# Kernel tuning notes

Hardware: AMD Instinct MI355X
Metric: run time of the kernel (lower is better)

The kernel has to match this reference:

```python
import jax, jax.numpy as jnp
import numpy as np

N, D = 2048, 1024
H, KV, HD = 16, 4, 64
REPEATS = H // KV
SCALE = HD ** -0.5


def setup_inputs() -> dict:
    key = jax.random.key(0)
    ks = jax.random.split(key, 6)
    x = jax.random.normal(ks[0], (N, D), dtype=jnp.float32)
    # rotary tables: cos/sin of interleaved-pair angles (llama-style view_as_complex)
    pos = jnp.arange(N, dtype=jnp.float32)[:, None]
    inv_freq = 1.0 / (10000.0 ** (jnp.arange(0, HD, 2, dtype=jnp.float32) / HD))
    ang = pos * inv_freq[None, :]  # (N, HD//2)
    freqs_cos = jnp.cos(ang)
    freqs_sin = jnp.sin(ang)
    s = 0.02
    Wq = jax.random.normal(ks[1], (D, H * HD), dtype=jnp.float32) * s
    Wk = jax.random.normal(ks[2], (D, KV * HD), dtype=jnp.float32) * s
    Wv = jax.random.normal(ks[3], (D, KV * HD), dtype=jnp.float32) * s
    Wo = jax.random.normal(ks[4], (H * HD, D), dtype=jnp.float32) * s
    return {"x": x, "freqs_cos": freqs_cos, "freqs_sin": freqs_sin,
            "Wq": Wq, "Wk": Wk, "Wv": Wv, "Wo": Wo}


def _rope(t, cos, sin):
    # t: (N, heads, HD); interleaved complex pairs (even=real, odd=imag)
    tr = t[..., 0::2]
    ti = t[..., 1::2]
    c = cos[:, None, :]
    s = sin[:, None, :]
    out_r = tr * c - ti * s
    out_i = tr * s + ti * c
    return jnp.stack([out_r, out_i], axis=-1).reshape(t.shape)


def reference(x, freqs_cos, freqs_sin, Wq, Wk, Wv, Wo):
    n = x.shape[0]
    xq = (x @ Wq).reshape(n, H, HD)
    xk = (x @ Wk).reshape(n, KV, HD)
    xv = (x @ Wv).reshape(n, KV, HD)
    xq = _rope(xq, freqs_cos, freqs_sin)
    xk = _rope(xk, freqs_cos, freqs_sin)
    # repeat_kv along head dim (GQA)
    k = jnp.repeat(xk, REPEATS, axis=1)  # (n, H, HD)
    v = jnp.repeat(xv, REPEATS, axis=1)
    # memory_efficient_attention with mask=None: full attention over token axis
    scores = jnp.einsum('nhd,mhd->hnm', xq, k) * SCALE
    attn = jax.nn.softmax(scores, axis=-1)
    out = jnp.einsum('hnm,mhd->nhd', attn, v)
    return out.reshape(n, H * HD) @ Wo
```

## Files before the change

### kernel.cpp

```cpp
#include <hip/hip_runtime.h>

#define N_TOK 2048
#define DMODEL 1024
#define NH 16
#define NKV 4
#define HDIM 64
#define SCALE_LOG2E 0.1803368801111204f

typedef __attribute__((ext_vector_type(8))) short short8;
typedef __attribute__((ext_vector_type(4))) float f32x4;
typedef __attribute__((ext_vector_type(16))) float f32x16;
typedef unsigned short u16;
typedef unsigned int u32;

__device__ __forceinline__ u16 f2bf(float x) {
    u32 u = __float_as_uint(x);
    u += 0x7FFF + ((u >> 16) & 1);
    return (u16)(u >> 16);
}
__device__ __forceinline__ u32 pack2(float a, float b) {
    return (u32)f2bf(a) | ((u32)f2bf(b) << 16);
}
__device__ __forceinline__ u32 pack2t(float a, float b) {
    return __builtin_amdgcn_perm(__float_as_uint(b), __float_as_uint(a), 0x07060302u);
}

__global__ __launch_bounds__(256) void prep(
    const float* __restrict__ Wq, const float* __restrict__ Wk,
    const float* __restrict__ Wv, const float* __restrict__ Wo,
    const float* __restrict__ x,
    u16* __restrict__ Wqt, u16* __restrict__ Wkt, u16* __restrict__ Wvt,
    u16* __restrict__ Wot, u16* __restrict__ xb)
{
    const int z = blockIdx.z;
    const int t = threadIdx.x;
    if (z == 4) {
        size_t base = ((size_t)(blockIdx.y * 16 + blockIdx.x)) * 8192;
#pragma unroll
        for (int i = 0; i < 8; ++i) {
            float4 v = *(const float4*)(x + base + i * 1024 + t * 4);
            uint2 p; p.x = pack2(v.x, v.y); p.y = pack2(v.z, v.w);
            *(uint2*)(xb + base + i * 1024 + t * 4) = p;
        }
        return;
    }
    const float* W; u16* Wt; int NC;
    if      (z == 0) { W = Wq; Wt = Wqt; NC = 1024; }
    else if (z == 1) { W = Wk; Wt = Wkt; NC = 256; }
    else if (z == 2) { W = Wv; Wt = Wvt; NC = 256; }
    else             { W = Wo; Wt = Wot; NC = 1024; }
    const int n0 = blockIdx.x * 64;
    if (n0 >= NC) return;
    const int k0 = blockIdx.y * 64;
    __shared__ float T[64][68];
    const int row = t >> 2, cs = (t & 3) * 16;
#pragma unroll
    for (int i = 0; i < 4; ++i)
        *(float4*)&T[row][cs + i * 4] =
            *(const float4*)(W + (size_t)(k0 + row) * NC + n0 + cs + i * 4);
    __syncthreads();
    const int nl = t >> 2, ks = (t & 3) * 16;
    u32 pk[8];
#pragma unroll
    for (int i = 0; i < 8; ++i)
        pk[i] = pack2(T[ks + 2 * i][nl], T[ks + 2 * i + 1][nl]);
    u16* dst = Wt + (size_t)(n0 + nl) * DMODEL + k0 + ks;
    uint4 w0; w0.x = pk[0]; w0.y = pk[1]; w0.z = pk[2]; w0.w = pk[3];
    uint4 w1; w1.x = pk[4]; w1.y = pk[5]; w1.z = pk[6]; w1.w = pk[7];
    *(uint4*)(dst) = w0;
    *(uint4*)(dst + 8) = w1;
}

__global__ __launch_bounds__(256, 2) void gemm_qkv(
    const u16* __restrict__ A,
    const u16* __restrict__ B0, const u16* __restrict__ B1, const u16* __restrict__ B2,
    u16* __restrict__ D0, u16* __restrict__ D1, u16* __restrict__ FVout,
    const float* __restrict__ fc, const float* __restrict__ fs)
{
    __shared__ u16 As[2][128][72];
    __shared__ u16 Bs[2][64][72];
    const int t = threadIdx.x;
    const int m0 = blockIdx.x * 128;
    const int by = blockIdx.y;

    const u16* Bt; int nl0, ep;
    u16* dbf = nullptr; int dstride = 0; float epsc = 1.f;
    if (by < 16)      { Bt = B0; nl0 = by * 64;        dbf = D0; ep = 1; dstride = 1024;
                        epsc = SCALE_LOG2E; }
    else if (by < 20) { Bt = B1; nl0 = (by - 16) * 64; dbf = D1; ep = 1; dstride = 256; }
    else              { Bt = B2; nl0 = (by - 20) * 64; ep = 2; }

    const int w = t >> 6, lane = t & 63;
    const int quad = lane >> 4, l15 = lane & 15;
    const int wm = (w >> 1) * 64, wn = (w & 1) * 32;
    const int arow = t >> 1, ac = (t & 1) * 32;
    const int brow = t >> 2, bc = (t & 3) * 16;

    const u16* Ap = A + (size_t)(m0 + arow) * DMODEL + ac;
    const u16* Bp = Bt + (size_t)(nl0 + brow) * DMODEL + bc;

    f32x4 acc[4][2];
#pragma unroll
    for (int i = 0; i < 4; ++i)
#pragma unroll
        for (int j = 0; j < 2; ++j) acc[i][j] = {0.f, 0.f, 0.f, 0.f};

    uint4 a_r[4], b_r[2];
#pragma unroll
    for (int ci = 0; ci < 4; ++ci) a_r[ci] = *(const uint4*)(Ap + ci * 8);
    b_r[0] = *(const uint4*)(Bp);
    b_r[1] = *(const uint4*)(Bp + 8);
#pragma unroll
    for (int ci = 0; ci < 4; ++ci) *(uint4*)&As[0][arow][ac + ci * 8] = a_r[ci];
    *(uint4*)&Bs[0][brow][bc]     = b_r[0];
    *(uint4*)&Bs[0][brow][bc + 8] = b_r[1];
    __syncthreads();

    for (int it = 0; it < 16; ++it) {
        const int cur = it & 1;
        const bool more = (it + 1) < 16;
        if (more) {
            const int k1 = (it + 1) * 64;
#pragma unroll
            for (int ci = 0; ci < 4; ++ci) a_r[ci] = *(const uint4*)(Ap + k1 + ci * 8);
            b_r[0] = *(const uint4*)(Bp + k1);
            b_r[1] = *(const uint4*)(Bp + k1 + 8);
        }
#pragma unroll
        for (int c = 0; c < 2; ++c) {
            short8 af[4], bf[2];
#pragma unroll
            for (int i = 0; i < 4; ++i)
                af[i] = *(const short8*)&As[cur][wm + i * 16 + l15][c * 32 + quad * 8];
#pragma unroll
            for (int j = 0; j < 2; ++j)
                bf[j] = *(const short8*)&Bs[cur][wn + j * 16 + l15][c * 32 + quad * 8];
#pragma unroll
            for (int i = 0; i < 4; ++i)
#pragma unroll
                for (int j = 0; j < 2; ++j)
                    acc[i][j] = __builtin_amdgcn_mfma_f32_16x16x32_bf16(af[i], bf[j], acc[i][j], 0, 0, 0);
        }
        if (more) {
            const int nx = cur ^ 1;
#pragma unroll
            for (int ci = 0; ci < 4; ++ci) *(uint4*)&As[nx][arow][ac + ci * 8] = a_r[ci];
            *(uint4*)&Bs[nx][brow][bc]     = b_r[0];
            *(uint4*)&Bs[nx][brow][bc + 8] = b_r[1];
            __syncthreads();
        }
    }

#pragma unroll
    for (int i = 0; i < 4; ++i)
#pragma unroll
        for (int j = 0; j < 2; ++j) {
            const int cl = nl0 + wn + j * 16 + l15;
            if (ep == 1) {
#pragma unroll
                for (int r4 = 0; r4 < 4; ++r4) {
                    const int r = m0 + wm + i * 16 + quad * 4 + r4;
                    float own = acc[i][j][r4];
                    float other = __shfl_xor(own, 1, 64);
                    const int p = (cl & 63) >> 1;
                    const float c = fc[r * 32 + p] * epsc, s = fs[r * 32 + p] * epsc;
                    float outv = ((cl & 1) == 0) ? (own * c - other * s)
                                                 : (other * s + own * c);
                    dbf[(size_t)r * dstride + cl] = f2bf(outv);
                }
            } else {
                const int rb = m0 + wm + i * 16 + quad * 4;
                const int g = cl >> 6, d = cl & 63;
                const int d2 = d >> 5, dl = d & 31;
                const int keyblk = rb >> 7, kg = (rb >> 5) & 3;
                const int kst = (rb >> 4) & 1, hb = (rb >> 3) & 1, jv = rb & 7;
                size_t idx = ((((((size_t)(g * 16 + keyblk) * 4 + kg) * 2 + kst) * 2 + d2)
                               * 2 + hb) * 32 + dl) * 8 + jv;
                uint2 pk;
                pk.x = pack2(acc[i][j][0], acc[i][j][1]);
                pk.y = pack2(acc[i][j][2], acc[i][j][3]);
                *(uint2*)(FVout + idx) = pk;
            }
        }
}

__global__ __launch_bounds__(256, 2) void gemm_out(
    const u16* __restrict__ A, const u16* __restrict__ Bt, float* __restrict__ Dout)
{
    __shared__ u16 As[2][64][72];
    __shared__ u16 Bs[2][64][72];
    const int t = threadIdx.x;
    const int m0 = blockIdx.x * 64;
    const int nl0 = blockIdx.y * 64;

    const int w = t >> 6, lane = t & 63;
    const int quad = lane >> 4, l15 = lane & 15;
    const int wm = (w >> 1) * 32, wn = (w & 1) * 32;
    const int srow = t >> 2, sk = (t & 3) * 16;

    const u16* Ap = A + (size_t)(m0 + srow) * DMODEL + sk;
    const u16* Bp = Bt + (size_t)(nl0 + srow) * DMODEL + sk;

    f32x4 acc[2][2];
#pragma unroll
    for (int i = 0; i < 2; ++i)
#pragma unroll
        for (int j = 0; j < 2; ++j) acc[i][j] = {0.f, 0.f, 0.f, 0.f};

    uint4 a_r[2], b_r[2];
    a_r[0] = *(const uint4*)(Ap);     a_r[1] = *(const uint4*)(Ap + 8);
    b_r[0] = *(const uint4*)(Bp);     b_r[1] = *(const uint4*)(Bp + 8);
    *(uint4*)&As[0][srow][sk]     = a_r[0];
    *(uint4*)&As[0][srow][sk + 8] = a_r[1];
    *(uint4*)&Bs[0][srow][sk]     = b_r[0];
    *(uint4*)&Bs[0][srow][sk + 8] = b_r[1];
    __syncthreads();

    for (int it = 0; it < 16; ++it) {
        const int cur = it & 1;
        const bool more = (it + 1) < 16;
        if (more) {
            const int k1 = (it + 1) * 64;
            a_r[0] = *(const uint4*)(Ap + k1);     a_r[1] = *(const uint4*)(Ap + k1 + 8);
            b_r[0] = *(const uint4*)(Bp + k1);     b_r[1] = *(const uint4*)(Bp + k1 + 8);
        }
#pragma unroll
        for (int c = 0; c < 2; ++c) {
            short8 af[2], bf[2];
#pragma unroll
            for (int i = 0; i < 2; ++i)
                af[i] = *(const short8*)&As[cur][wm + i * 16 + l15][c * 32 + quad * 8];
#pragma unroll
            for (int j = 0; j < 2; ++j)
                bf[j] = *(const short8*)&Bs[cur][wn + j * 16 + l15][c * 32 + quad * 8];
#pragma unroll
            for (int i = 0; i < 2; ++i)
#pragma unroll
                for (int j = 0; j < 2; ++j)
                    acc[i][j] = __builtin_amdgcn_mfma_f32_16x16x32_bf16(af[i], bf[j], acc[i][j], 0, 0, 0);
        }
        if (more) {
            const int nx = cur ^ 1;
            *(uint4*)&As[nx][srow][sk]     = a_r[0];
            *(uint4*)&As[nx][srow][sk + 8] = a_r[1];
            *(uint4*)&Bs[nx][srow][sk]     = b_r[0];
            *(uint4*)&Bs[nx][srow][sk + 8] = b_r[1];
            __syncthreads();
        }
    }

#pragma unroll
    for (int i = 0; i < 2; ++i)
#pragma unroll
        for (int j = 0; j < 2; ++j) {
            const int cl = nl0 + wn + j * 16 + l15;
#pragma unroll
            for (int r4 = 0; r4 < 4; ++r4) {
                const int r = m0 + wm + i * 16 + quad * 4 + r4;
                Dout[(size_t)r * 1024 + cl] = acc[i][j][r4];
            }
        }
}

__global__ __launch_bounds__(256, 2) void attn(
    const u16* __restrict__ Qb, const u16* __restrict__ Kb,
    const u16* __restrict__ FV, u16* __restrict__ Ob)
{
    __shared__ u16 Ks[2][2][64][72];
    __shared__ u16 Ps[4][32][40];

    const int t = threadIdx.x;
    const int n0 = blockIdx.x * 64;
    const int h = blockIdx.y, kvh = h >> 2;
    const int w = t >> 6, lane = t & 63;
    const int hi = lane >> 5, l31 = lane & 31;
    const int qgrp = w & 1, khalf = w >> 1;
    const int srow = t >> 1, ssel = (t & 1) * 32;
    const int khalf_s = srow >> 6, klocal = srow & 63;

    const short8 ones = {(short)0x3F80, (short)0x3F80, (short)0x3F80, (short)0x3F80,
                         (short)0x3F80, (short)0x3F80, (short)0x3F80, (short)0x3F80};

    const u16* qp = Qb + (size_t)(n0 + qgrp * 32 + l31) * (NH * HDIM) + h * HDIM + hi * 8;
    short8 qf[4];
#pragma unroll
    for (int s = 0; s < 4; ++s) qf[s] = *(const short8*)(qp + s * 16);

    const u16* kbase = Kb + (size_t)(khalf_s * 1024 + klocal) * (NKV * HDIM) + kvh * HDIM + ssel;
    const u16* fvb = FV + ((size_t)kvh * 16 * 8192) + (size_t)lane * 8;

    f32x16 o[2], o_l;
#pragma unroll
    for (int d2 = 0; d2 < 2; ++d2)
#pragma unroll
        for (int r = 0; r < 16; ++r) o[d2][r] = 0.f;
#pragma unroll
    for (int r = 0; r < 16; ++r) o_l[r] = 0.f;

#pragma unroll
    for (int c = 0; c < 4; ++c)
        *(uint4*)&Ks[0][khalf_s][klocal][ssel + c * 8] = *(const uint4*)(kbase + c * 8);
    __syncthreads();

    for (int rd = 0; rd < 16; ++rd) {
        const int cur = rd & 1, nxt = cur ^ 1;
        const int rdn = (rd + 1) & 15;
        uint4 kr[4];
#pragma unroll
        for (int c = 0; c < 4; ++c)
            kr[c] = *(const uint4*)(kbase + (size_t)(rdn * 64) * (NKV * HDIM) + c * 8);

#pragma unroll
        for (int kg = 0; kg < 2; ++kg) {
            const int kg_global = khalf * 32 + rd * 2 + kg;
            const int keyblk = kg_global >> 2, kgi = kg_global & 3;
            short8 vf[2][2];
#pragma unroll
            for (int s = 0; s < 2; ++s)
#pragma unroll
                for (int d2 = 0; d2 < 2; ++d2)
                    vf[s][d2] = *(const short8*)(fvb +
                        ((((size_t)keyblk * 4 + kgi) * 2 + s) * 2 + d2) * 512);
            f32x16 sa;
#pragma unroll
            for (int r = 0; r < 16; ++r) sa[r] = 0.f;
#pragma unroll
            for (int s = 0; s < 4; ++s) {
                short8 kf = *(const short8*)&Ks[cur][khalf][kg * 32 + l31][s * 16 + hi * 8];
                sa = __builtin_amdgcn_mfma_f32_32x32x16_bf16(kf, qf[s], sa, 0, 0, 0);
            }
            float p[16];
#pragma unroll
            for (int r = 0; r < 16; ++r) p[r] = __builtin_amdgcn_exp2f(sa[r]);
#pragma unroll
            for (int blk = 0; blk < 4; ++blk) {
                uint2 pk;
                pk.x = pack2t(p[blk * 4 + 0], p[blk * 4 + 1]);
                pk.y = pack2t(p[blk * 4 + 2], p[blk * 4 + 3]);
                *(uint2*)&Ps[w][l31][blk * 8 + 4 * hi] = pk;
            }
            const short8 ap0 = *(const short8*)&Ps[w][l31][hi * 8];
            const short8 ap1 = *(const short8*)&Ps[w][l31][16 + hi * 8];
#pragma unroll
            for (int d2 = 0; d2 < 2; ++d2) {
                o[d2] = __builtin_amdgcn_mfma_f32_32x32x16_bf16(ap0, vf[0][d2], o[d2], 0, 0, 0);
                o[d2] = __builtin_amdgcn_mfma_f32_32x32x16_bf16(ap1, vf[1][d2], o[d2], 0, 0, 0);
            }
            o_l = __builtin_amdgcn_mfma_f32_32x32x16_bf16(ap0, ones, o_l, 0, 0, 0);
            o_l = __builtin_amdgcn_mfma_f32_32x32x16_bf16(ap1, ones, o_l, 0, 0, 0);
        }
#pragma unroll
        for (int c = 0; c < 4; ++c)
            *(uint4*)&Ks[nxt][khalf_s][klocal][ssel + c * 8] = kr[c];
        __syncthreads();
    }

    float* Xf = (float*)&Ks[0][0][0][0];
    if (khalf == 1) {
#pragma unroll
        for (int d2 = 0; d2 < 2; ++d2)
#pragma unroll
            for (int r = 0; r < 16; ++r) {
                const int q32 = (r & 3) + 8 * (r >> 2) + 4 * hi;
                Xf[qgrp * 2048 + q32 * 64 + d2 * 32 + l31] = o[d2][r];
            }
        if (l31 == 0) {
#pragma unroll
            for (int r = 0; r < 16; ++r) {
                const int q32 = (r & 3) + 8 * (r >> 2) + 4 * hi;
                Xf[4096 + qgrp * 32 + q32] = o_l[r];
            }
        }
    }
    __syncthreads();
    if (khalf == 0) {
        float linv[16];
#pragma unroll
        for (int r = 0; r < 16; ++r) {
            const int q32 = (r & 3) + 8 * (r >> 2) + 4 * hi;
            linv[r] = 1.f / (o_l[r] + Xf[4096 + qgrp * 32 + q32]);
        }
#pragma unroll
        for (int d2 = 0; d2 < 2; ++d2)
#pragma unroll
            for (int r = 0; r < 16; ++r) {
                const int q32 = (r & 3) + 8 * (r >> 2) + 4 * hi;
                const float val = o[d2][r] + Xf[qgrp * 2048 + q32 * 64 + d2 * 32 + l31];
                const int qrow = n0 + qgrp * 32 + q32;
                Ob[(size_t)qrow * (NH * HDIM) + h * HDIM + d2 * 32 + l31] = f2bf(val * linv[r]);
            }
    }
}

extern "C" void kernel_launch(void* const* d_in, const int* in_sizes, int n_in,
                              void* d_out, int out_size, void* d_ws, size_t ws_size,
                              hipStream_t stream) {
    const float* x  = (const float*)d_in[0];
    const float* fc = (const float*)d_in[1];
    const float* fs = (const float*)d_in[2];
    const float* Wq = (const float*)d_in[3];
    const float* Wk = (const float*)d_in[4];
    const float* Wv = (const float*)d_in[5];
    const float* Wo = (const float*)d_in[6];
    float* out = (float*)d_out;

    u16* ws  = (u16*)d_ws;
    u16* xb  = ws;
    u16* Wqt = xb  + (size_t)2048 * 1024;
    u16* Wkt = Wqt + (size_t)1024 * 1024;
    u16* Wvt = Wkt + (size_t)256 * 1024;
    u16* Wot = Wvt + (size_t)256 * 1024;
    u16* qb  = Wot + (size_t)1024 * 1024;
    u16* kb  = qb  + (size_t)2048 * 1024;
    u16* fv  = kb  + (size_t)2048 * 256;
    u16* aob = fv  + (size_t)256 * 2048;

    prep<<<dim3(16, 16, 5), dim3(256), 0, stream>>>(Wq, Wk, Wv, Wo, x,
                                                    Wqt, Wkt, Wvt, Wot, xb);
    gemm_qkv<<<dim3(16, 24), dim3(256), 0, stream>>>(xb, Wqt, Wkt, Wvt,
                                                     qb, kb, fv, fc, fs);
    attn<<<dim3(32, 16), dim3(256), 0, stream>>>(qb, kb, fv, aob);
    gemm_out<<<dim3(32, 16), dim3(256), 0, stream>>>(aob, Wot, out);
}
```

Baseline: 137.2 us.

## Fuse four kernels into one persistent kernel with grid-wide barriers

Measured after the change: 350.7 us. +155.5%, slower.

```diff
diff --git a/kernel.cpp b/kernel.cpp
--- a/kernel.cpp
+++ b/kernel.cpp
@@ -6,6 +6,7 @@
 #define NKV 4
 #define HDIM 64
 #define SCALE_LOG2E 0.1803368801111204f
+#define NBLK 512
 
 typedef __attribute__((ext_vector_type(8))) short short8;
 typedef __attribute__((ext_vector_type(4))) float f32x4;
@@ -25,369 +26,382 @@
     return __builtin_amdgcn_perm(__float_as_uint(b), __float_as_uint(a), 0x07060302u);
 }
 
-__global__ __launch_bounds__(256) void prep(
+__device__ __forceinline__ void gridbar(u32* cnt, u32* gen) {
+    __syncthreads();
+    if (threadIdx.x == 0) {
+        __threadfence();
+        u32 g = __hip_atomic_load(gen, __ATOMIC_RELAXED, __HIP_MEMORY_SCOPE_AGENT);
+        if (__hip_atomic_fetch_add(cnt, 1u, __ATOMIC_ACQ_REL, __HIP_MEMORY_SCOPE_AGENT)
+            == (u32)(NBLK - 1)) {
+            __hip_atomic_store(cnt, 0u, __ATOMIC_RELAXED, __HIP_MEMORY_SCOPE_AGENT);
+            __hip_atomic_fetch_add(gen, 1u, __ATOMIC_RELEASE, __HIP_MEMORY_SCOPE_AGENT);
+        } else {
+            while (__hip_atomic_load(gen, __ATOMIC_RELAXED, __HIP_MEMORY_SCOPE_AGENT) == g)
+                __builtin_amdgcn_s_sleep(2);
+        }
+        __threadfence();
+    }
+    __syncthreads();
+}
+
+__global__ __launch_bounds__(256, 2) void fused(
+    const float* __restrict__ x, const float* __restrict__ fc, const float* __restrict__ fs,
     const float* __restrict__ Wq, const float* __restrict__ Wk,
     const float* __restrict__ Wv, const float* __restrict__ Wo,
-    const float* __restrict__ x,
-    u16* __restrict__ Wqt, u16* __restrict__ Wkt, u16* __restrict__ Wvt,
-    u16* __restrict__ Wot, u16* __restrict__ xb)
+    u16* __restrict__ xb, u16* __restrict__ Wqt, u16* __restrict__ Wkt,
+    u16* __restrict__ Wvt, u16* __restrict__ Wot,
+    u16* __restrict__ qb, u16* __restrict__ kb, u16* __restrict__ fv,
+    u16* __restrict__ aob, float* __restrict__ out, u32* __restrict__ sync)
 {
-    const int z = blockIdx.z;
+    __shared__ __align__(16) unsigned char smem[55296];
+    const int b = blockIdx.x;
     const int t = threadIdx.x;
-    if (z == 4) {
-        size_t base = ((size_t)(blockIdx.y * 16 + blockIdx.x)) * 8192;
-#pragma unroll
-        for (int i = 0; i < 8; ++i) {
-            float4 v = *(const float4*)(x + base + i * 1024 + t * 4);
-            uint2 p; p.x = pack2(v.x, v.y); p.y = pack2(v.z, v.w);
-            *(uint2*)(xb + base + i * 1024 + t * 4) = p;
-        }
-        return;
+
+    for (int job = b; job < 896; job += NBLK) {
+        if (job < 256) {
+            size_t base = (size_t)job * 8192;
+#pragma unroll
+            for (int i = 0; i < 8; ++i) {
+                float4 v = *(const float4*)(x + base + i * 1024 + t * 4);
+                uint2 p; p.x = pack2(v.x, v.y); p.y = pack2(v.z, v.w);
+                *(uint2*)(xb + base + i * 1024 + t * 4) = p;
+            }
+        } else {
+            const float* W; u16* Wt; int NC, jr;
+            if (job < 512)      { W = Wq; Wt = Wqt; NC = 1024; jr = job - 256; }
+            else if (job < 768) { W = Wo; Wt = Wot; NC = 1024; jr = job - 512; }
+            else if (job < 832) { W = Wk; Wt = Wkt; NC = 256;  jr = job - 768; }
+            else                { W = Wv; Wt = Wvt; NC = 256;  jr = job - 832; }
+            const int n0 = (NC == 1024 ? (jr & 15) : (jr & 3)) * 64;
+            const int k0 = (NC == 1024 ? (jr >> 4) : (jr >> 2)) * 64;
+            float (*T)[68] = (float(*)[68])smem;
+            const int row = t >> 2, cs = (t & 3) * 16;
+#pragma unroll
+            for (int i = 0; i < 4; ++i)
+                *(float4*)&T[row][cs + i * 4] =
+                    *(const float4*)(W + (size_t)(k0 + row) * NC + n0 + cs + i * 4);
+            __syncthreads();
+            const int nl = t >> 2, ks = (t & 3) * 16;
+            u32 pk[8];
+#pragma unroll
+            for (int i = 0; i < 8; ++i)
+                pk[i] = pack2(T[ks + 2 * i][nl], T[ks + 2 * i + 1][nl]);
+            u16* dst = Wt + (size_t)(n0 + nl) * DMODEL + k0 + ks;
+            uint4 w0; w0.x = pk[0]; w0.y = pk[1]; w0.z = pk[2]; w0.w = pk[3];
+            uint4 w1; w1.x = pk[4]; w1.y = pk[5]; w1.z = pk[6]; w1.w = pk[7];
+            *(uint4*)(dst) = w0;
+            *(uint4*)(dst + 8) = w1;
+            __syncthreads();
+        }
     }
-    const float* W; u16* Wt; int NC;
-    if      (z == 0) { W = Wq; Wt = Wqt; NC = 1024; }
-    else if (z == 1) { W = Wk; Wt = Wkt; NC = 256; }
-    else if (z == 2) { W = Wv; Wt = Wvt; NC = 256; }
-    else             { W = Wo; Wt = Wot; NC = 1024; }
-    const int n0 = blockIdx.x * 64;
-    if (n0 >= NC) return;
-    const int k0 = blockIdx.y * 64;
-    __shared__ float T[64][68];
-    const int row = t >> 2, cs = (t & 3) * 16;
-#pragma unroll
-    for (int i = 0; i < 4; ++i)
-        *(float4*)&T[row][cs + i * 4] =
-            *(const float4*)(W + (size_t)(k0 + row) * NC + n0 + cs + i * 4);
-    __syncthreads();
-    const int nl = t >> 2, ks = (t & 3) * 16;
-    u32 pk[8];
-#pragma unroll
-    for (int i = 0; i < 8; ++i)
-        pk[i] = pack2(T[ks + 2 * i][nl], T[ks + 2 * i + 1][nl]);
-    u16* dst = Wt + (size_t)(n0 + nl) * DMODEL + k0 + ks;
-    uint4 w0; w0.x = pk[0]; w0.y = pk[1]; w0.z = pk[2]; w0.w = pk[3];
-    uint4 w1; w1.x = pk[4]; w1.y = pk[5]; w1.z = pk[6]; w1.w = pk[7];
-    *(uint4*)(dst) = w0;
-    *(uint4*)(dst + 8) = w1;
-}
-
-__global__ __launch_bounds__(256, 2) void gemm_qkv(
-    const u16* __restrict__ A,
-    const u16* __restrict__ B0, const u16* __restrict__ B1, const u16* __restrict__ B2,
-    u16* __restrict__ D0, u16* __restrict__ D1, u16* __restrict__ FVout,
-    const float* __restrict__ fc, const float* __restrict__ fs)
-{
-    __shared__ u16 As[2][128][72];
-    __shared__ u16 Bs[2][64][72];
-    const int t = threadIdx.x;
-    const int m0 = blockIdx.x * 128;
-    const int by = blockIdx.y;
-
-    const u16* Bt; int nl0, ep;
-    u16* dbf = nullptr; int dstride = 0; float epsc = 1.f;
-    if (by < 16)      { Bt = B0; nl0 = by * 64;        dbf = D0; ep = 1; dstride = 1024;
-                        epsc = SCALE_LOG2E; }
-    else if (by < 20) { Bt = B1; nl0 = (by - 16) * 64; dbf = D1; ep = 1; dstride = 256; }
-    else              { Bt = B2; nl0 = (by - 20) * 64; ep = 2; }
-
-    const int w = t >> 6, lane = t & 63;
-    const int quad = lane >> 4, l15 = lane & 15;
-    const int wm = (w >> 1) * 64, wn = (w & 1) * 32;
-    const int arow = t >> 1, ac = (t & 1) * 32;
-    const int brow = t >> 2, bc = (t & 3) * 16;
-
-    const u16* Ap = A + (size_t)(m0 + arow) * DMODEL + ac;
-    const u16* Bp = Bt + (size_t)(nl0 + brow) * DMODEL + bc;
-
-    f32x4 acc[4][2];
-#pragma unroll
-    for (int i = 0; i < 4; ++i)
-#pragma unroll
-        for (int j = 0; j < 2; ++j) acc[i][j] = {0.f, 0.f, 0.f, 0.f};
-
-    uint4 a_r[4], b_r[2];
-#pragma unroll
-    for (int ci = 0; ci < 4; ++ci) a_r[ci] = *(const uint4*)(Ap + ci * 8);
-    b_r[0] = *(const uint4*)(Bp);
-    b_r[1] = *(const uint4*)(Bp + 8);
-#pragma unroll
-    for (int ci = 0; ci < 4; ++ci) *(uint4*)&As[0][arow][ac + ci * 8] = a_r[ci];
-    *(uint4*)&Bs[0][brow][bc]     = b_r[0];
-    *(uint4*)&Bs[0][brow][bc + 8] = b_r[1];
-    __syncthreads();
-
-    for (int it = 0; it < 16; ++it) {
-        const int cur = it & 1;
-        const bool more = (it + 1) < 16;
-        if (more) {
-            const int k1 = (it + 1) * 64;
-#pragma unroll
-            for (int ci = 0; ci < 4; ++ci) a_r[ci] = *(const uint4*)(Ap + k1 + ci * 8);
-            b_r[0] = *(const uint4*)(Bp + k1);
-            b_r[1] = *(const uint4*)(Bp + k1 + 8);
-        }
-#pragma unroll
-        for (int c = 0; c < 2; ++c) {
-            short8 af[4], bf[2];
-#pragma unroll
-            for (int i = 0; i < 4; ++i)
-                af[i] = *(const short8*)&As[cur][wm + i * 16 + l15][c * 32 + quad * 8];
-#pragma unroll
-            for (int j = 0; j < 2; ++j)
-                bf[j] = *(const short8*)&Bs[cur][wn + j * 16 + l15][c * 32 + quad * 8];
-#pragma unroll
-            for (int i = 0; i < 4; ++i)
+    gridbar(sync, sync + 16);
+
+    if (b < 384) {
+        u16 (*As)[128][72] = (u16(*)[128][72])smem;
+        u16 (*Bs)[64][72]  = (u16(*)[64][72])(smem + 36864);
+        const int m0 = (b & 15) * 128;
+        const int by = b >> 4;
+
+        const u16* Bt; int nl0, ep;
+        u16* dbf = nullptr; int dstride = 0; float epsc = 1.f;
+        if (by < 16)      { Bt = Wqt; nl0 = by * 64;        dbf = qb; ep = 1; dstride = 1024;
+                            epsc = SCALE_LOG2E; }
+        else if (by < 20) { Bt = Wkt; nl0 = (by - 16) * 64; dbf = kb; ep = 1; dstride = 256; }
+        else              { Bt = Wvt; nl0 = (by - 20) * 64; ep = 2; }
+
+        const int w = t >> 6, lane = t & 63;
+        const int quad = lane >> 4, l15 = lane & 15;
+        const int wm = (w >> 1) * 64, wn = (w & 1) * 32;
+        const int arow = t >> 1, ac = (t & 1) * 32;
+        const int brow = t >> 2, bc = (t & 3) * 16;
+
+        const u16* Ap = xb + (size_t)(m0 + arow) * DMODEL + ac;
+        const u16* Bp = Bt + (size_t)(nl0 + brow) * DMODEL + bc;
+
+        f32x4 acc[4][2];
+#pragma unroll
+        for (int i = 0; i < 4; ++i)
+#pragma unroll
+            for (int j = 0; j < 2; ++j) acc[i][j] = {0.f, 0.f, 0.f, 0.f};
+
+        uint4 a_r[4], b_r[2];
+#pragma unroll
+        for (int ci = 0; ci < 4; ++ci) a_r[ci] = *(const uint4*)(Ap + ci * 8);
+        b_r[0] = *(const uint4*)(Bp);
+        b_r[1] = *(const uint4*)(Bp + 8);
+#pragma unroll
+        for (int ci = 0; ci < 4; ++ci) *(uint4*)&As[0][arow][ac + ci * 8] = a_r[ci];
+        *(uint4*)&Bs[0][brow][bc]     = b_r[0];
+        *(uint4*)&Bs[0][brow][bc + 8] = b_r[1];
+        __syncthreads();
+
+        for (int it = 0; it < 16; ++it) {
+            const int cur = it & 1;
+            const bool more = (it + 1) < 16;
+            if (more) {
+                const int k1 = (it + 1) * 64;
+#pragma unroll
+                for (int ci = 0; ci < 4; ++ci) a_r[ci] = *(const uint4*)(Ap + k1 + ci * 8);
+                b_r[0] = *(const uint4*)(Bp + k1);
+                b_r[1] = *(const uint4*)(Bp + k1 + 8);
+            }
+#pragma unroll
+            for (int c = 0; c < 2; ++c) {
+                short8 af[4], bf[2];
+#pragma unroll
+                for (int i = 0; i < 4; ++i)
+                    af[i] = *(const short8*)&As[cur][wm + i * 16 + l15][c * 32 + quad * 8];
 #pragma unroll
                 for (int j = 0; j < 2; ++j)
-                    acc[i][j] = __builtin_amdgcn_mfma_f32_16x16x32_bf16(af[i], bf[j], acc[i][j], 0, 0, 0);
-        }
-        if (more) {
-            const int nx = cur ^ 1;
-#pragma unroll
-            for (int ci = 0; ci < 4; ++ci) *(uint4*)&As[nx][arow][ac + ci * 8] = a_r[ci];
-            *(uint4*)&Bs[nx][brow][bc]     = b_r[0];
-            *(uint4*)&Bs[nx][brow][bc + 8] = b_r[1];
+                    bf[j] = *(const short8*)&Bs[cur][wn + j * 16 + l15][c * 32 + quad * 8];
+#pragma unroll
+                for (int i = 0; i < 4; ++i)
+#pragma unroll
+                    for (int j = 0; j < 2; ++j)
+                        acc[i][j] = __builtin_amdgcn_mfma_f32_16x16x32_bf16(af[i], bf[j], acc[i][j], 0, 0, 0);
+            }
+            if (more) {
+                const int nx = cur ^ 1;
+#pragma unroll
+                for (int ci = 0; ci < 4; ++ci) *(uint4*)&As[nx][arow][ac + ci * 8] = a_r[ci];
+                *(uint4*)&Bs[nx][brow][bc]     = b_r[0];
+                *(uint4*)&Bs[nx][brow][bc + 8] = b_r[1];
+                __syncthreads();
+            }
+        }
+
+#pragma unroll
+        for (int i = 0; i < 4; ++i)
+#pragma unroll
+            for (int j = 0; j < 2; ++j) {
+                const int cl = nl0 + wn + j * 16 + l15;
+                if (ep == 1) {
+#pragma unroll
+                    for (int r4 = 0; r4 < 4; ++r4) {
+                        const int r = m0 + wm + i * 16 + quad * 4 + r4;
+                        float own = acc[i][j][r4];
+                        float other = __shfl_xor(own, 1, 64);
+                        const int p = (cl & 63) >> 1;
+                        const float c = fc[r * 32 + p] * epsc, s = fs[r * 32 + p] * epsc;
+                        float outv = ((cl & 1) == 0) ? (own * c - other * s)
+                                                     : (other * s + own * c);
+                        dbf[(size_t)r * dstride + cl] = f2bf(outv);
+                    }
+                } else {
+                    const int rb = m0 + wm + i * 16 + quad * 4;
+                    const int g = cl >> 6, d = cl & 63;
+                    const int d2 = d >> 5, dl = d & 31;
+                    const int keyblk = rb >> 7, kg = (rb >> 5) & 3;
+                    const int kst = (rb >> 4) & 1, hb = (rb >> 3) & 1, jv = rb & 7;
+                    size_t idx = ((((((size_t)(g * 16 + keyblk) * 4 + kg) * 2 + kst) * 2 + d2)
+                                   * 2 + hb) * 32 + dl) * 8 + jv;
+                    uint2 pk;
+                    pk.x = pack2(acc[i][j][0], acc[i][j][1]);
+                    pk.y = pack2(acc[i][j][2], acc[i][j][3]);
+                    *(uint2*)(fv + idx) = pk;
+                }
+            }
+    }
+    gridbar(sync, sync + 16);
+
+    {
+        u16 (*Ks)[2][64][72] = (u16(*)[2][64][72])smem;
+        u16 (*Ps)[32][40]    = (u16(*)[32][40])(smem + 36864);
+        const int n0 = (b & 31) * 64;
+        const int h = b >> 5, kvh = h >> 2;
+        const int w = t >> 6, lane = t & 63;
+        const int hi = lane >> 5, l31 = lane & 31;
+        const int qgrp = w & 1, khalf = w >> 1;
+        const int srow = t >> 1, ssel = (t & 1) * 32;
+        const int khalf_s = srow >> 6, klocal = srow & 63;
+
+        const short8 ones = {(short)0x3F80, (short)0x3F80, (short)0x3F80, (short)0x3F80,
+                             (short)0x3F80, (short)0x3F80, (short)0x3F80, (short)0x3F80};
+
+        const u16* qp = qb + (size_t)(n0 + qgrp * 32 + l31) * (NH * HDIM) + h * HDIM + hi * 8;
+        short8 qf[4];
+#pragma unroll
+        for (int s = 0; s < 4; ++s) qf[s] = *(const short8*)(qp + s * 16);
+
+        const u16* kbase = kb + (size_t)(khalf_s * 1024 + klocal) * (NKV * HDIM) + kvh * HDIM + ssel;
+        const u16* fvb = fv + ((size_t)kvh * 16 * 8192) + (size_t)lane * 8;
+
+        f32x16 o[2], o_l;
+#pragma unroll
+        for (int d2 = 0; d2 < 2; ++d2)
+#pragma unroll
+            for (int r = 0; r < 16; ++r) o[d2][r] = 0.f;
+#pragma unroll
+        for (int r = 0; r < 16; ++r) o_l[r] = 0.f;
+
+#pragma unroll
+        for (int c = 0; c < 4; ++c)
+            *(uint4*)&Ks[0][khalf_s][klocal][ssel + c * 8] = *(const uint4*)(kbase + c * 8);
+        __syncthreads();
+
+        for (int rd = 0; rd < 16; ++rd) {
+            const int cur = rd & 1, nxt = cur ^ 1;
+            const int rdn = (rd + 1) & 15;
+            uint4 kr[4];
+#pragma unroll
+            for (int c = 0; c < 4; ++c)
+                kr[c] = *(const uint4*)(kbase + (size_t)(rdn * 64) * (NKV * HDIM) + c * 8);
+
+#pragma unroll
+            for (int kg = 0; kg < 2; ++kg) {
+                const int kg_global = khalf * 32 + rd * 2 + kg;
+                const int keyblk = kg_global >> 2, kgi = kg_global & 3;
+                short8 vf[2][2];
+#pragma unroll
+                for (int s = 0; s < 2; ++s)
+#pragma unroll
+                    for (int d2 = 0; d2 < 2; ++d2)
+                        vf[s][d2] = *(const short8*)(fvb +
+                            ((((size_t)keyblk * 4 + kgi) * 2 + s) * 2 + d2) * 512);
+                f32x16 sa;
+#pragma unroll
+                for (int r = 0; r < 16; ++r) sa[r] = 0.f;
+#pragma unroll
+                for (int s = 0; s < 4; ++s) {
+                    short8 kf = *(const short8*)&Ks[cur][khalf][kg * 32 + l31][s * 16 + hi * 8];
+                    sa = __builtin_amdgcn_mfma_f32_32x32x16_bf16(kf, qf[s], sa, 0, 0, 0);
+                }
+                float p[16];
+#pragma unroll
+                for (int r = 0; r < 16; ++r) p[r] = __builtin_amdgcn_exp2f(sa[r]);
+#pragma unroll
+                for (int blk = 0; blk < 4; ++blk) {
+                    uint2 pk;
+                    pk.x = pack2t(p[blk * 4 + 0], p[blk * 4 + 1]);
+                    pk.y = pack2t(p[blk * 4 + 2], p[blk * 4 + 3]);
+                    *(uint2*)&Ps[w][l31][blk * 8 + 4 * hi] = pk;
+                }
+                const short8 ap0 = *(const short8*)&Ps[w][l31][hi * 8];
+                const short8 ap1 = *(const short8*)&Ps[w][l31][16 + hi * 8];
+#pragma unroll
+                for (int d2 = 0; d2 < 2; ++d2) {
+                    o[d2] = __builtin_amdgcn_mfma_f32_32x32x16_bf16(ap0, vf[0][d2], o[d2], 0, 0, 0);
+                    o[d2] = __builtin_amdgcn_mfma_f32_32x32x16_bf16(ap1, vf[1][d2], o[d2], 0, 0, 0);
+                }
+                o_l = __builtin_amdgcn_mfma_f32_32x32x16_bf16(ap0, ones, o_l, 0, 0, 0);
+                o_l = __builtin_amdgcn_mfma_f32_32x32x16_bf16(ap1, ones, o_l, 0, 0, 0);
+            }
+#pragma unroll
+            for (int c = 0; c < 4; ++c)
+                *(uint4*)&Ks[nxt][khalf_s][klocal][ssel + c * 8] = kr[c];
             __syncthreads();
         }
+
+        float* Xf = (float*)smem;
+        if (khalf == 1) {
+#pragma unroll
+            for (int d2 = 0; d2 < 2; ++d2)
+#pragma unroll
+                for (int r = 0; r < 16; ++r) {
+                    const int q32 = (r & 3) + 8 * (r >> 2) + 4 * hi;
+                    Xf[qgrp * 2048 + q32 * 64 + d2 * 32 + l31] = o[d2][r];
+                }
+            if (l31 == 0) {
+#pragma unroll
+                for (int r = 0; r < 16; ++r) {
+                    const int q32 = (r & 3) + 8 * (r >> 2) + 4 * hi;
+                    Xf[4096 + qgrp * 32 + q32] = o_l[r];
+                }
+            }
+        }
+        __syncthreads();
+        if (khalf == 0) {
+            float linv[16];
+#pragma unroll
+            for (int r = 0; r < 16; ++r) {
+                const int q32 = (r & 3) + 8 * (r >> 2) + 4 * hi;
+                linv[r] = 1.f / (o_l[r] + Xf[4096 + qgrp * 32 + q32]);
+            }
+#pragma unroll
+            for (int d2 = 0; d2 < 2; ++d2)
+#pragma unroll
+                for (int r = 0; r < 16; ++r) {
+                    const int q32 = (r & 3) + 8 * (r >> 2) + 4 * hi;
+                    const float val = o[d2][r] + Xf[qgrp * 2048 + q32 * 64 + d2 * 32 + l31];
+                    const int qrow = n0 + qgrp * 32 + q32;
+                    aob[(size_t)qrow * (NH * HDIM) + h * HDIM + d2 * 32 + l31] = f2bf(val * linv[r]);
+                }
+        }
     }
-
-#pragma unroll
-    for (int i = 0; i < 4; ++i)
-#pragma unroll
-        for (int j = 0; j < 2; ++j) {
-            const int cl = nl0 + wn + j * 16 + l15;
-            if (ep == 1) {
+    gridbar(sync, sync + 16);
+
+    {
+        u16 (*As)[64][72] = (u16(*)[64][72])smem;
+        u16 (*Bs)[64][72] = (u16(*)[64][72])(smem + 18432);
+        const int m0 = (b & 31) * 64;
+        const int nl0 = (b >> 5) * 64;
+
+        const int w = t >> 6, lane = t & 63;
+        const int quad = lane >> 4, l15 = lane & 15;
+        const int wm = (w >> 1) * 32, wn = (w & 1) * 32;
+        const int srow = t >> 2, sk = (t & 3) * 16;
+
+        const u16* Ap = aob + (size_t)(m0 + srow) * DMODEL + sk;
+        const u16* Bp = Wot + (size_t)(nl0 + srow) * DMODEL + sk;
+
+        f32x4 acc[2][2];
+#pragma unroll
+        for (int i = 0; i < 2; ++i)
+#pragma unroll
+            for (int j = 0; j < 2; ++j) acc[i][j] = {0.f, 0.f, 0.f, 0.f};
+
+        uint4 a_r[2], b_r[2];
+        a_r[0] = *(const uint4*)(Ap);     a_r[1] = *(const uint4*)(Ap + 8);
+        b_r[0] = *(const uint4*)(Bp);     b_r[1] = *(const uint4*)(Bp + 8);
+        *(uint4*)&As[0][srow][sk]     = a_r[0];
+        *(uint4*)&As[0][srow][sk + 8] = a_r[1];
+        *(uint4*)&Bs[0][srow][sk]     = b_r[0];
+        *(uint4*)&Bs[0][srow][sk + 8] = b_r[1];
+        __syncthreads();
+
+        for (int it = 0; it < 16; ++it) {
+            const int cur = it & 1;
+            const bool more = (it + 1) < 16;
+            if (more) {
+                const int k1 = (it + 1) * 64;
+                a_r[0] = *(const uint4*)(Ap + k1);     a_r[1] = *(const uint4*)(Ap + k1 + 8);
+                b_r[0] = *(const uint4*)(Bp + k1);     b_r[1] = *(const uint4*)(Bp + k1 + 8);
+            }
+#pragma unroll
+            for (int c = 0; c < 2; ++c) {
+                short8 af[2], bf[2];
+#pragma unroll
+                for (int i = 0; i < 2; ++i)
+                    af[i] = *(const short8*)&As[cur][wm + i * 16 + l15][c * 32 + quad * 8];
+#pragma unroll
+                for (int j = 0; j < 2; ++j)
+                    bf[j] = *(const short8*)&Bs[cur][wn + j * 16 + l15][c * 32 + quad * 8];
+#pragma unroll
+                for (int i = 0; i < 2; ++i)
+#pragma unroll
+                    for (int j = 0; j < 2; ++j)
+                        acc[i][j] = __builtin_amdgcn_mfma_f32_16x16x32_bf16(af[i], bf[j], acc[i][j], 0, 0, 0);
+            }
+            if (more) {
+                const int nx = cur ^ 1;
+                *(uint4*)&As[nx][srow][sk]     = a_r[0];
+                *(uint4*)&As[nx][srow][sk + 8] = a_r[1];
+                *(uint4*)&Bs[nx][srow][sk]     = b_r[0];
+                *(uint4*)&Bs[nx][srow][sk + 8] = b_r[1];
+                __syncthreads();
+            }
+        }
+
+#pragma unroll
+        for (int i = 0; i < 2; ++i)
+#pragma unroll
+            for (int j = 0; j < 2; ++j) {
+                const int cl = nl0 + wn + j * 16 + l15;
 #pragma unroll
                 for (int r4 = 0; r4 < 4; ++r4) {
                     const int r = m0 + wm + i * 16 + quad * 4 + r4;
-                    float own = acc[i][j][r4];
-                    float other = __shfl_xor(own, 1, 64);
-                    const int p = (cl & 63) >> 1;
-                    const float c = fc[r * 32 + p] * epsc, s = fs[r * 32 + p] * epsc;
-                    float outv = ((cl & 1) == 0) ? (own * c - other * s)
-                                                 : (other * s + own * c);
-                    dbf[(size_t)r * dstride + cl] = f2bf(outv);
-                }
-            } else {
-                const int rb = m0 + wm + i * 16 + quad * 4;
-                const int g = cl >> 6, d = cl & 63;
-                const int d2 = d >> 5, dl = d & 31;
-                const int keyblk = rb >> 7, kg = (rb >> 5) & 3;
-                const int kst = (rb >> 4) & 1, hb = (rb >> 3) & 1, jv = rb & 7;
-                size_t idx = ((((((size_t)(g * 16 + keyblk) * 4 + kg) * 2 + kst) * 2 + d2)
-                               * 2 + hb) * 32 + dl) * 8 + jv;
-                uint2 pk;
-                pk.x = pack2(acc[i][j][0], acc[i][j][1]);
-                pk.y = pack2(acc[i][j][2], acc[i][j][3]);
-                *(uint2*)(FVout + idx) = pk;
-            }
-        }
-}
-
-__global__ __launch_bounds__(256, 2) void gemm_out(
-    const u16* __restrict__ A, const u16* __restrict__ Bt, float* __restrict__ Dout)
-{
-    __shared__ u16 As[2][64][72];
-    __shared__ u16 Bs[2][64][72];
-    const int t = threadIdx.x;
-    const int m0 = blockIdx.x * 64;
-    const int nl0 = blockIdx.y * 64;
-
-    const int w = t >> 6, lane = t & 63;
-    const int quad = lane >> 4, l15 = lane & 15;
-    const int wm = (w >> 1) * 32, wn = (w & 1) * 32;
-    const int srow = t >> 2, sk = (t & 3) * 16;
-
-    const u16* Ap = A + (size_t)(m0 + srow) * DMODEL + sk;
-    const u16* Bp = Bt + (size_t)(nl0 + srow) * DMODEL + sk;
-
-    f32x4 acc[2][2];
-#pragma unroll
-    for (int i = 0; i < 2; ++i)
-#pragma unroll
-        for (int j = 0; j < 2; ++j) acc[i][j] = {0.f, 0.f, 0.f, 0.f};
-
-    uint4 a_r[2], b_r[2];
-    a_r[0] = *(const uint4*)(Ap);     a_r[1] = *(const uint4*)(Ap + 8);
-    b_r[0] = *(const uint4*)(Bp);     b_r[1] = *(const uint4*)(Bp + 8);
-    *(uint4*)&As[0][srow][sk]     = a_r[0];
-    *(uint4*)&As[0][srow][sk + 8] = a_r[1];
-    *(uint4*)&Bs[0][srow][sk]     = b_r[0];
-    *(uint4*)&Bs[0][srow][sk + 8] = b_r[1];
-    __syncthreads();
-
-    for (int it = 0; it < 16; ++it) {
-        const int cur = it & 1;
-        const bool more = (it + 1) < 16;
-        if (more) {
-            const int k1 = (it + 1) * 64;
-            a_r[0] = *(const uint4*)(Ap + k1);     a_r[1] = *(const uint4*)(Ap + k1 + 8);
-            b_r[0] = *(const uint4*)(Bp + k1);     b_r[1] = *(const uint4*)(Bp + k1 + 8);
-        }
-#pragma unroll
-        for (int c = 0; c < 2; ++c) {
-            short8 af[2], bf[2];
-#pragma unroll
-            for (int i = 0; i < 2; ++i)
-                af[i] = *(const short8*)&As[cur][wm + i * 16 + l15][c * 32 + quad * 8];
-#pragma unroll
-            for (int j = 0; j < 2; ++j)
-                bf[j] = *(const short8*)&Bs[cur][wn + j * 16 + l15][c * 32 + quad * 8];
-#pragma unroll
-            for (int i = 0; i < 2; ++i)
-#pragma unroll
-                for (int j = 0; j < 2; ++j)
-                    acc[i][j] = __builtin_amdgcn_mfma_f32_16x16x32_bf16(af[i], bf[j], acc[i][j], 0, 0, 0);
-        }
-        if (more) {
-            const int nx = cur ^ 1;
-            *(uint4*)&As[nx][srow][sk]     = a_r[0];
-            *(uint4*)&As[nx][srow][sk + 8] = a_r[1];
-            *(uint4*)&Bs[nx][srow][sk]     = b_r[0];
-            *(uint4*)&Bs[nx][srow][sk + 8] = b_r[1];
-            __syncthreads();
-        }
-    }
-
-#pragma unroll
-    for (int i = 0; i < 2; ++i)
-#pragma unroll
-        for (int j = 0; j < 2; ++j) {
-            const int cl = nl0 + wn + j * 16 + l15;
-#pragma unroll
-            for (int r4 = 0; r4 < 4; ++r4) {
-                const int r = m0 + wm + i * 16 + quad * 4 + r4;
-                Dout[(size_t)r * 1024 + cl] = acc[i][j][r4];
-            }
-        }
-}
-
-__global__ __launch_bounds__(256, 2) void attn(
-    const u16* __restrict__ Qb, const u16* __restrict__ Kb,
-    const u16* __restrict__ FV, u16* __restrict__ Ob)
-{
-    __shared__ u16 Ks[2][2][64][72];
-    __shared__ u16 Ps[4][32][40];
-
-    const int t = threadIdx.x;
-    const int n0 = blockIdx.x * 64;
-    const int h = blockIdx.y, kvh = h >> 2;
-    const int w = t >> 6, lane = t & 63;
-    const int hi = lane >> 5, l31 = lane & 31;
-    const int qgrp = w & 1, khalf = w >> 1;
-    const int srow = t >> 1, ssel = (t & 1) * 32;
-    const int khalf_s = srow >> 6, klocal = srow & 63;
-
-    const short8 ones = {(short)0x3F80, (short)0x3F80, (short)0x3F80, (short)0x3F80,
-                         (short)0x3F80, (short)0x3F80, (short)0x3F80, (short)0x3F80};
-
-    const u16* qp = Qb + (size_t)(n0 + qgrp * 32 + l31) * (NH * HDIM) + h * HDIM + hi * 8;
-    short8 qf[4];
-#pragma unroll
-    for (int s = 0; s < 4; ++s) qf[s] = *(const short8*)(qp + s * 16);
-
-    const u16* kbase = Kb + (size_t)(khalf_s * 1024 + klocal) * (NKV * HDIM) + kvh * HDIM + ssel;
-    const u16* fvb = FV + ((size_t)kvh * 16 * 8192) + (size_t)lane * 8;
-
-    f32x16 o[2], o_l;
-#pragma unroll
-    for (int d2 = 0; d2 < 2; ++d2)
-#pragma unroll
-        for (int r = 0; r < 16; ++r) o[d2][r] = 0.f;
-#pragma unroll
-    for (int r = 0; r < 16; ++r) o_l[r] = 0.f;
-
-#pragma unroll
-    for (int c = 0; c < 4; ++c)
-        *(uint4*)&Ks[0][khalf_s][klocal][ssel + c * 8] = *(const uint4*)(kbase + c * 8);
-    __syncthreads();
-
-    for (int rd = 0; rd < 16; ++rd) {
-        const int cur = rd & 1, nxt = cur ^ 1;
-        const int rdn = (rd + 1) & 15;
-        uint4 kr[4];
-#pragma unroll
-        for (int c = 0; c < 4; ++c)
-            kr[c] = *(const uint4*)(kbase + (size_t)(rdn * 64) * (NKV * HDIM) + c * 8);
-
-#pragma unroll
-        for (int kg = 0; kg < 2; ++kg) {
-            const int kg_global = khalf * 32 + rd * 2 + kg;
-            const int keyblk = kg_global >> 2, kgi = kg_global & 3;
-            short8 vf[2][2];
-#pragma unroll
-            for (int s = 0; s < 2; ++s)
-#pragma unroll
-                for (int d2 = 0; d2 < 2; ++d2)
-                    vf[s][d2] = *(const short8*)(fvb +
-                        ((((size_t)keyblk * 4 + kgi) * 2 + s) * 2 + d2) * 512);
-            f32x16 sa;
-#pragma unroll
-            for (int r = 0; r < 16; ++r) sa[r] = 0.f;
-#pragma unroll
-            for (int s = 0; s < 4; ++s) {
-                short8 kf = *(const short8*)&Ks[cur][khalf][kg * 32 + l31][s * 16 + hi * 8];
-                sa = __builtin_amdgcn_mfma_f32_32x32x16_bf16(kf, qf[s], sa, 0, 0, 0);
-            }
-            float p[16];
-#pragma unroll
-            for (int r = 0; r < 16; ++r) p[r] = __builtin_amdgcn_exp2f(sa[r]);
-#pragma unroll
-            for (int blk = 0; blk < 4; ++blk) {
-                uint2 pk;
-                pk.x = pack2t(p[blk * 4 + 0], p[blk * 4 + 1]);
-                pk.y = pack2t(p[blk * 4 + 2], p[blk * 4 + 3]);
-                *(uint2*)&Ps[w][l31][blk * 8 + 4 * hi] = pk;
-            }
-            const short8 ap0 = *(const short8*)&Ps[w][l31][hi * 8];
-            const short8 ap1 = *(const short8*)&Ps[w][l31][16 + hi * 8];
-#pragma unroll
-            for (int d2 = 0; d2 < 2; ++d2) {
-                o[d2] = __builtin_amdgcn_mfma_f32_32x32x16_bf16(ap0, vf[0][d2], o[d2], 0, 0, 0);
-                o[d2] = __builtin_amdgcn_mfma_f32_32x32x16_bf16(ap1, vf[1][d2], o[d2], 0, 0, 0);
-            }
-            o_l = __builtin_amdgcn_mfma_f32_32x32x16_bf16(ap0, ones, o_l, 0, 0, 0);
-            o_l = __builtin_amdgcn_mfma_f32_32x32x16_bf16(ap1, ones, o_l, 0, 0, 0);
-        }
-#pragma unroll
-        for (int c = 0; c < 4; ++c)
-            *(uint4*)&Ks[nxt][khalf_s][klocal][ssel + c * 8] = kr[c];
-        __syncthreads();
-    }
-
-    float* Xf = (float*)&Ks[0][0][0][0];
-    if (khalf == 1) {
-#pragma unroll
-        for (int d2 = 0; d2 < 2; ++d2)
-#pragma unroll
-            for (int r = 0; r < 16; ++r) {
-                const int q32 = (r & 3) + 8 * (r >> 2) + 4 * hi;
-                Xf[qgrp * 2048 + q32 * 64 + d2 * 32 + l31] = o[d2][r];
-            }
-        if (l31 == 0) {
-#pragma unroll
-            for (int r = 0; r < 16; ++r) {
-                const int q32 = (r & 3) + 8 * (r >> 2) + 4 * hi;
-                Xf[4096 + qgrp * 32 + q32] = o_l[r];
-            }
-        }
-    }
-    __syncthreads();
-    if (khalf == 0) {
-        float linv[16];
-#pragma unroll
-        for (int r = 0; r < 16; ++r) {
-            const int q32 = (r & 3) + 8 * (r >> 2) + 4 * hi;
-            linv[r] = 1.f / (o_l[r] + Xf[4096 + qgrp * 32 + q32]);
-        }
-#pragma unroll
-        for (int d2 = 0; d2 < 2; ++d2)
-#pragma unroll
-            for (int r = 0; r < 16; ++r) {
-                const int q32 = (r & 3) + 8 * (r >> 2) + 4 * hi;
-                const float val = o[d2][r] + Xf[qgrp * 2048 + q32 * 64 + d2 * 32 + l31];
-                const int qrow = n0 + qgrp * 32 + q32;
-                Ob[(size_t)qrow * (NH * HDIM) + h * HDIM + d2 * 32 + l31] = f2bf(val * linv[r]);
+                    out[(size_t)r * 1024 + cl] = acc[i][j][r4];
+                }
             }
     }
 }
@@ -414,11 +428,10 @@
     u16* kb  = qb  + (size_t)2048 * 1024;
     u16* fv  = kb  + (size_t)2048 * 256;
     u16* aob = fv  + (size_t)256 * 2048;
-
-    prep<<<dim3(16, 16, 5), dim3(256), 0, stream>>>(Wq, Wk, Wv, Wo, x,
-                                                    Wqt, Wkt, Wvt, Wot, xb);
-    gemm_qkv<<<dim3(16, 24), dim3(256), 0, stream>>>(xb, Wqt, Wkt, Wvt,
-                                                     qb, kb, fv, fc, fs);
-    attn<<<dim3(32, 16), dim3(256), 0, stream>>>(qb, kb, fv, aob);
-    gemm_out<<<dim3(32, 16), dim3(256), 0, stream>>>(aob, Wot, out);
-}
+    u32* sync = (u32*)(aob + (size_t)2048 * 1024);
+
+    hipMemsetAsync(sync, 0, 128, stream);
+    fused<<<dim3(NBLK), dim3(256), 0, stream>>>(x, fc, fs, Wq, Wk, Wv, Wo,
+                                                xb, Wqt, Wkt, Wvt, Wot,
+                                                qb, kb, fv, aob, out, sync);
+}
```

## Use direct global-to-LDS loads with XOR swizzle and smaller QKV tiles

Applied to the files above, without the earlier changes.

Result: no change. 138.5 us (+0.9%).

```diff
diff --git a/kernel.cpp b/kernel.cpp
--- a/kernel.cpp
+++ b/kernel.cpp
@@ -23,6 +23,12 @@
 }
 __device__ __forceinline__ u32 pack2t(float a, float b) {
     return __builtin_amdgcn_perm(__float_as_uint(b), __float_as_uint(a), 0x07060302u);
+}
+
+__device__ __forceinline__ void gload16(const u16* g, u16* l) {
+    __builtin_amdgcn_global_load_lds(
+        (const __attribute__((address_space(1))) unsigned int*)g,
+        (__attribute__((address_space(3))) unsigned int*)l, 16, 0, 0);
 }
 
 __global__ __launch_bounds__(256) void prep(
@@ -71,16 +77,16 @@
     *(uint4*)(dst + 8) = w1;
 }
 
-__global__ __launch_bounds__(256, 2) void gemm_qkv(
+__global__ __launch_bounds__(256, 3) void gemm_qkv(
     const u16* __restrict__ A,
     const u16* __restrict__ B0, const u16* __restrict__ B1, const u16* __restrict__ B2,
     u16* __restrict__ D0, u16* __restrict__ D1, u16* __restrict__ FVout,
     const float* __restrict__ fc, const float* __restrict__ fs)
 {
-    __shared__ u16 As[2][128][72];
-    __shared__ u16 Bs[2][64][72];
+    __shared__ u16 As[2][64][64];
+    __shared__ u16 Bs[2][64][64];
     const int t = threadIdx.x;
-    const int m0 = blockIdx.x * 128;
+    const int m0 = blockIdx.x * 64;
     const int by = blockIdx.y;
 
     const u16* Bt; int nl0, ep;
@@ -92,67 +98,57 @@
 
     const int w = t >> 6, lane = t & 63;
     const int quad = lane >> 4, l15 = lane & 15;
-    const int wm = (w >> 1) * 64, wn = (w & 1) * 32;
-    const int arow = t >> 1, ac = (t & 1) * 32;
-    const int brow = t >> 2, bc = (t & 3) * 16;
-
-    const u16* Ap = A + (size_t)(m0 + arow) * DMODEL + ac;
-    const u16* Bp = Bt + (size_t)(nl0 + brow) * DMODEL + bc;
-
-    f32x4 acc[4][2];
-#pragma unroll
-    for (int i = 0; i < 4; ++i)
+    const int wm = (w >> 1) * 32, wn = (w & 1) * 32;
+    const int rx = l15 & 7;
+
+    const int sro = w * 16 + (lane >> 3);
+    const int sco = ((lane & 7) ^ (lane >> 3)) * 8;
+    const u16* ApL = A + (size_t)(m0 + sro) * DMODEL + sco;
+    const u16* BpL = Bt + (size_t)(nl0 + sro) * DMODEL + sco;
+
+    f32x4 acc[2][2];
+#pragma unroll
+    for (int i = 0; i < 2; ++i)
 #pragma unroll
         for (int j = 0; j < 2; ++j) acc[i][j] = {0.f, 0.f, 0.f, 0.f};
 
-    uint4 a_r[4], b_r[2];
-#pragma unroll
-    for (int ci = 0; ci < 4; ++ci) a_r[ci] = *(const uint4*)(Ap + ci * 8);
-    b_r[0] = *(const uint4*)(Bp);
-    b_r[1] = *(const uint4*)(Bp + 8);
-#pragma unroll
-    for (int ci = 0; ci < 4; ++ci) *(uint4*)&As[0][arow][ac + ci * 8] = a_r[ci];
-    *(uint4*)&Bs[0][brow][bc]     = b_r[0];
-    *(uint4*)&Bs[0][brow][bc + 8] = b_r[1];
+#pragma unroll
+    for (int k = 0; k < 2; ++k) {
+        gload16(ApL + k * 8 * DMODEL, &As[0][w * 16 + k * 8][0]);
+        gload16(BpL + k * 8 * DMODEL, &Bs[0][w * 16 + k * 8][0]);
+    }
     __syncthreads();
 
     for (int it = 0; it < 16; ++it) {
         const int cur = it & 1;
-        const bool more = (it + 1) < 16;
-        if (more) {
-            const int k1 = (it + 1) * 64;
-#pragma unroll
-            for (int ci = 0; ci < 4; ++ci) a_r[ci] = *(const uint4*)(Ap + k1 + ci * 8);
-            b_r[0] = *(const uint4*)(Bp + k1);
-            b_r[1] = *(const uint4*)(Bp + k1 + 8);
+        if (it + 1 < 16) {
+            const int kk = (it + 1) * 64;
+#pragma unroll
+            for (int k = 0; k < 2; ++k) {
+                gload16(ApL + k * 8 * DMODEL + kk, &As[cur ^ 1][w * 16 + k * 8][0]);
+                gload16(BpL + k * 8 * DMODEL + kk, &Bs[cur ^ 1][w * 16 + k * 8][0]);
+            }
         }
 #pragma unroll
         for (int c = 0; c < 2; ++c) {
-            short8 af[4], bf[2];
-#pragma unroll
-            for (int i = 0; i < 4; ++i)
-                af[i] = *(const short8*)&As[cur][wm + i * 16 + l15][c * 32 + quad * 8];
+            short8 af[2], bf[2];
+#pragma unroll
+            for (int i = 0; i < 2; ++i)
+                af[i] = *(const short8*)&As[cur][wm + i * 16 + l15][((4 * c + quad) ^ rx) * 8];
 #pragma unroll
             for (int j = 0; j < 2; ++j)
-                bf[j] = *(const short8*)&Bs[cur][wn + j * 16 + l15][c * 32 + quad * 8];
-#pragma unroll
-            for (int i = 0; i < 4; ++i)
+                bf[j] = *(const short8*)&Bs[cur][wn + j * 16 + l15][((4 * c + quad) ^ rx) * 8];
+#pragma unroll
+            for (int i = 0; i < 2; ++i)
 #pragma unroll
                 for (int j = 0; j < 2; ++j)
                     acc[i][j] = __builtin_amdgcn_mfma_f32_16x16x32_bf16(af[i], bf[j], acc[i][j], 0, 0, 0);
         }
-        if (more) {
-            const int nx = cur ^ 1;
-#pragma unroll
-            for (int ci = 0; ci < 4; ++ci) *(uint4*)&As[nx][arow][ac + ci * 8] = a_r[ci];
-            *(uint4*)&Bs[nx][brow][bc]     = b_r[0];
-            *(uint4*)&Bs[nx][brow][bc + 8] = b_r[1];
-            __syncthreads();
-        }
-    }
-
-#pragma unroll
-    for (int i = 0; i < 4; ++i)
+        __syncthreads();
+    }
+
+#pragma unroll
+    for (int i = 0; i < 2; ++i)
 #pragma unroll
         for (int j = 0; j < 2; ++j) {
             const int cl = nl0 + wn + j * 16 + l15;
@@ -187,8 +183,8 @@
 __global__ __launch_bounds__(256, 2) void gemm_out(
     const u16* __restrict__ A, const u16* __restrict__ Bt, float* __restrict__ Dout)
 {
-    __shared__ u16 As[2][64][72];
-    __shared__ u16 Bs[2][64][72];
+    __shared__ u16 As[2][64][64];
+    __shared__ u16 Bs[2][64][64];
     const int t = threadIdx.x;
     const int m0 = blockIdx.x * 64;
     const int nl0 = blockIdx.y * 64;
@@ -196,10 +192,12 @@
     const int w = t >> 6, lane = t & 63;
     const int quad = lane >> 4, l15 = lane & 15;
     const int wm = (w >> 1) * 32, wn = (w & 1) * 32;
-    const int srow = t >> 2, sk = (t & 3) * 16;
-
-    const u16* Ap = A + (size_t)(m0 + srow) * DMODEL + sk;
-    const u16* Bp = Bt + (size_t)(nl0 + srow) * DMODEL + sk;
+    const int rx = l15 & 7;
+
+    const int sro = w * 16 + (lane >> 3);
+    const int sco = ((lane & 7) ^ (lane >> 3)) * 8;
+    const u16* ApL = A + (size_t)(m0 + sro) * DMODEL + sco;
+    const u16* BpL = Bt + (size_t)(nl0 + sro) * DMODEL + sco;
 
     f32x4 acc[2][2];
 #pragma unroll
@@ -207,46 +205,39 @@
 #pragma unroll
         for (int j = 0; j < 2; ++j) acc[i][j] = {0.f, 0.f, 0.f, 0.f};
 
-    uint4 a_r[2], b_r[2];
-    a_r[0] = *(const uint4*)(Ap);     a_r[1] = *(const uint4*)(Ap + 8);
-    b_r[0] = *(const uint4*)(Bp);     b_r[1] = *(const uint4*)(Bp + 8);
-    *(uint4*)&As[0][srow][sk]     = a_r[0];
-    *(uint4*)&As[0][srow][sk + 8] = a_r[1];
-    *(uint4*)&Bs[0][srow][sk]     = b_r[0];
-    *(uint4*)&Bs[0][srow][sk + 8] = b_r[1];
+#pragma unroll
+    for (int k = 0; k < 2; ++k) {
+        gload16(ApL + k * 8 * DMODEL, &As[0][w * 16 + k * 8][0]);
+        gload16(BpL + k * 8 * DMODEL, &Bs[0][w * 16 + k * 8][0]);
+    }
     __syncthreads();
 
     for (int it = 0; it < 16; ++it) {
         const int cur = it & 1;
-        const bool more = (it + 1) < 16;
-        if (more) {
-            const int k1 = (it + 1) * 64;
-            a_r[0] = *(const uint4*)(Ap + k1);     a_r[1] = *(const uint4*)(Ap + k1 + 8);
-            b_r[0] = *(const uint4*)(Bp + k1);     b_r[1] = *(const uint4*)(Bp + k1 + 8);
+        if (it + 1 < 16) {
+            const int kk = (it + 1) * 64;
+#pragma unroll
+            for (int k = 0; k < 2; ++k) {
+                gload16(ApL + k * 8 * DMODEL + kk, &As[cur ^ 1][w * 16 + k * 8][0]);
+                gload16(BpL + k * 8 * DMODEL + kk, &Bs[cur ^ 1][w * 16 + k * 8][0]);
+            }
         }
 #pragma unroll
         for (int c = 0; c < 2; ++c) {
             short8 af[2], bf[2];
 #pragma unroll
             for (int i = 0; i < 2; ++i)
-                af[i] = *(const short8*)&As[cur][wm + i * 16 + l15][c * 32 + quad * 8];
+                af[i] = *(const short8*)&As[cur][wm + i * 16 + l15][((4 * c + quad) ^ rx) * 8];
 #pragma unroll
             for (int j = 0; j < 2; ++j)
-                bf[j] = *(const short8*)&Bs[cur][wn + j * 16 + l15][c * 32 + quad * 8];
+                bf[j] = *(const short8*)&Bs[cur][wn + j * 16 + l15][((4 * c + quad) ^ rx) * 8];
 #pragma unroll
             for (int i = 0; i < 2; ++i)
 #pragma unroll
                 for (int j = 0; j < 2; ++j)
                     acc[i][j] = __builtin_amdgcn_mfma_f32_16x16x32_bf16(af[i], bf[j], acc[i][j], 0, 0, 0);
         }
-        if (more) {
-            const int nx = cur ^ 1;
-            *(uint4*)&As[nx][srow][sk]     = a_r[0];
-            *(uint4*)&As[nx][srow][sk + 8] = a_r[1];
-            *(uint4*)&Bs[nx][srow][sk]     = b_r[0];
-            *(uint4*)&Bs[nx][srow][sk + 8] = b_r[1];
-            __syncthreads();
-        }
+        __syncthreads();
     }
 
 #pragma unroll
@@ -417,7 +408,7 @@
 
     prep<<<dim3(16, 16, 5), dim3(256), 0, stream>>>(Wq, Wk, Wv, Wo, x,
                                                     Wqt, Wkt, Wvt, Wot, xb);
-    gemm_qkv<<<dim3(16, 24), dim3(256), 0, stream>>>(xb, Wqt, Wkt, Wvt,
+    gemm_qkv<<<dim3(32, 24), dim3(256), 0, stream>>>(xb, Wqt, Wkt, Wvt,
                                                      qb, kb, fv, fc, fs);
     attn<<<dim3(32, 16), dim3(256), 0, stream>>>(qb, kb, fv, aob);
     gemm_out<<<dim3(32, 16), dim3(256), 0, stream>>>(aob, Wot, out);
```
